# Kernel optimization log

Measured on AMD Instinct MI355X. Metric: run time of the kernel, lower is better.

Reference implementation:

```python
import jax, jax.numpy as jnp
import numpy as np

B, S = 16, 768
DCOG, DENV, NENV = 64, 32, 8
D, N, L, FF, NC = 512, 64, 6, 2048, 1
DIL = (1, 2, 4, 8)
EPS = 1e-5


def _layer_norm(x, g, b):
    m = x.mean(-1, keepdims=True)
    v = ((x - m) ** 2).mean(-1, keepdims=True)
    return (x - m) * jax.lax.rsqrt(v + EPS) * g + b


def _conv1d(x, w, b, d):
    # x: (B, D, S), w: (O, I, K); 'same' padding = (K-1)*d//2 = d for K=3
    y = jax.lax.conv_general_dilated(x, w, (1,), [(d, d)], rhs_dilation=(d,),
                                     dimension_numbers=('NCH', 'OIH', 'NCH'))
    return y + b[None, :, None]


def _combine(c1, c2):
    a1, b1 = c1
    a2, b2 = c2
    return a1 * a2, a2 * b1 + b2


def _forward(x_cog, cw1, cb1, cw2, cb2, env_emb, ew1, eb1, ew2, eb2,
             fw1, fb1, fw2, fb2, pos_enc, conv_w, conv_b, wm_w, wm_b,
             ssm_w, ssm_b, A_log, ffw1, ffb1, ffw2, ffb2,
             g1, be1, g2, be2, pw1, pb1, pw2, pb2, x_env):
    # Dual-channel feature processor (dropout = identity at eval)
    z = x_cog / jnp.maximum(jnp.linalg.norm(x_cog, axis=-1, keepdims=True), 1e-12)
    z = jnp.maximum(z @ cw1 + cb1, 0.0) @ cw2 + cb2
    e = env_emb[x_env].mean(-2)                      # (B,S,NENV,D) -> (B,S,D)
    e = jnp.maximum(e @ ew1 + eb1, 0.0) @ ew2 + eb2
    hf = jnp.concatenate([z, e], -1)
    hf = jnp.maximum(hf @ fw1 + fb1, 0.0) @ fw2 + fb2
    h = hf + pos_enc[:S][None]

    def layer_step(h, p):
        cw, cb, wmw, wmb, sw, sb, alog, w1, b1, w2, b2, g1_, be1_, g2_, be2_ = p
        # Multi-scale dilated conv
        xt = h.transpose(0, 2, 1)                    # (B, D, S)
        outs = [_conv1d(xt, cw[i], cb[i], DIL[i]) for i in range(4)]
        alpha = jax.nn.softmax(xt.mean(-1) @ wmw + wmb, -1)   # (B, 4)
        hm = sum(alpha[:, i, None, None] * outs[i] for i in range(4)).transpose(0, 2, 1)
        h1 = _layer_norm(hm + h, g1_, be1_)
        # Selective state-space (diagonal A), parallel associative scan
        proj = jnp.einsum('bsd,kdn->kbsn', h1, sw) + sb[:, None, None, :]
        delta, Bt, Ct = jax.nn.softplus(proj[0]), proj[1], proj[2]
        a = jnp.exp(alog[None, None, :] * delta)     # (B, S, N)
        bu = Bt * h1[..., :N]
        _, hs = jax.lax.associative_scan(_combine, (a, bu), axis=1)
        y = jnp.sum(Ct * hs, -1, keepdims=True)      # (B, S, 1)
        h2 = _layer_norm(y + h1, g2_, be2_)          # broadcast over D, as in torch
        return jnp.maximum(h2 @ w1 + b1, 0.0) @ w2 + b2 + h2, None

    h, _ = jax.lax.scan(layer_step, h, (conv_w, conv_b, wm_w, wm_b, ssm_w, ssm_b,
                                        A_log, ffw1, ffb1, ffw2, ffb2, g1, be1, g2, be2))
    hg = h.mean(1)                                   # adaptive avg pool over S
    return jnp.maximum(hg @ pw1 + pb1, 0.0) @ pw2 + pb2


def setup_inputs():
    ks = iter(jax.random.split(jax.random.key(0), 48))
    def rn(shape, s=0.02):
        return jax.random.normal(next(ks), shape, jnp.float32) * s
    return {
        'x_cog': rn((B, S, DCOG), 1.0),
        'cw1': rn((DCOG, D)), 'cb1': jnp.zeros(D), 'cw2': rn((D, D)), 'cb2': jnp.zeros(D),
        'env_emb': rn((DENV, D), 1.0),
        'ew1': rn((D, D)), 'eb1': jnp.zeros(D), 'ew2': rn((D, D)), 'eb2': jnp.zeros(D),
        'fw1': rn((2 * D, D)), 'fb1': jnp.zeros(D), 'fw2': rn((D, D)), 'fb2': jnp.zeros(D),
        'pos_enc': rn((1000, D), 1.0),
        'conv_w': rn((L, 4, D, D, 3)), 'conv_b': jnp.zeros((L, 4, D)),
        'wm_w': rn((L, D, 4)), 'wm_b': jnp.zeros((L, 4)),
        'ssm_w': rn((L, 3, D, N)), 'ssm_b': jnp.zeros((L, 3, N)),
        'A_log': -jnp.abs(rn((L, N), 1.0)),
        'ffw1': rn((L, D, FF)), 'ffb1': jnp.zeros((L, FF)),
        'ffw2': rn((L, FF, D)), 'ffb2': jnp.zeros((L, D)),
        'g1': jnp.ones((L, D)), 'be1': jnp.zeros((L, D)),
        'g2': jnp.ones((L, D)), 'be2': jnp.zeros((L, D)),
        'pw1': rn((D, D // 2)), 'pb1': jnp.zeros(D // 2),
        'pw2': rn((D // 2, NC)), 'pb2': jnp.zeros(NC),
        'x_env': jax.random.randint(next(ks), (B, S, NENV), 0, DENV, jnp.int32),
    }


def reference(x_cog, cw1, cb1, cw2, cb2, env_emb, ew1, eb1, ew2, eb2,
              fw1, fb1, fw2, fb2, pos_enc, conv_w, conv_b, wm_w, wm_b,
              ssm_w, ssm_b, A_log, ffw1, ffb1, ffw2, ffb2,
              g1, be1, g2, be2, pw1, pb1, pw2, pb2, x_env):
    return _forward(x_cog, cw1, cb1, cw2, cb2, env_emb, ew1, eb1, ew2, eb2,
                    fw1, fb1, fw2, fb2, pos_enc, conv_w, conv_b, wm_w, wm_b,
                    ssm_w, ssm_b, A_log, ffw1, ffb1, ffw2, ffb2,
                    g1, be1, g2, be2, pw1, pb1, pw2, pb2, x_env)
```

## Files before the change

### kernel.cpp

```cpp
#include <hip/hip_runtime.h>
#include <cstdint>
#include <cstddef>

namespace {

constexpr int B = 16, S = 768, BS = B * S, D = 512, FF = 2048, L = 6;
constexpr float EPS = 1e-5f;

typedef float f32x4 __attribute__((ext_vector_type(4)));
typedef _Float16 f16x8 __attribute__((ext_vector_type(8)));

__device__ __forceinline__ float wave_sum(float v) {
#pragma unroll
  for (int o = 32; o > 0; o >>= 1) v += __shfl_xor(v, o, 64);
  return v;
}

__device__ __forceinline__ short f16b(float x) {
  const _Float16 h = (_Float16)x;
  return __builtin_bit_cast(short, h);
}
__device__ __forceinline__ float h2f(short s) {
  return (float)__builtin_bit_cast(_Float16, s);
}

__device__ __forceinline__ void gload16(const void* g, void* l) {
  __builtin_amdgcn_global_load_lds(
      (const __attribute__((address_space(1))) void*)g,
      (__attribute__((address_space(3))) void*)l, 16, 0, 0);
}


template <bool RELU, bool PACK>
__global__ __launch_bounds__(256, 3) void gemm_h(
    const short* __restrict__ A, int lda, const short* __restrict__ Wt,
    int ldw, int Klen, const float* __restrict__ bias,
    short* __restrict__ ph, int ldp) {
  __shared__ alignas(16) short sAh[8192], sBh[8192];
  const int tid = threadIdx.x;
  const unsigned Nt = gridDim.x;
  const unsigned lin = blockIdx.y * Nt + blockIdx.x;
  const unsigned cpx = (Nt * gridDim.y) >> 3;
  const unsigned swz = (lin & 7) * cpx + (lin >> 3);
  const int bn = (int)(swz % Nt) * 128, bm = (int)(swz / Nt) * 128;
  const int wave = tid >> 6, lane = tid & 63;
  const int wr = (wave >> 1) * 64, wc = (wave & 1) * 64;
  const int lr = lane & 15, sl = lane >> 4;
  const short* Ab = A + (size_t)bm * lda;
  const short* Wb = Wt + (size_t)bn * ldw;
  f32x4 acc[4][4] = {};
  for (int kk = 0; kk < Klen; kk += 64) {
#pragma unroll
    for (int jj = 0; jj < 4; ++jj) {
      const int G = jj * 256 + tid;
      const int srow = G >> 3, sl0 = G & 7;
      const int gsl = sl0 ^ (srow & 7);
      const int dst = G * 8;
      gload16(Ab + (size_t)srow * lda + kk + gsl * 8, &sAh[dst]);
      gload16(Wb + (size_t)srow * ldw + kk + gsl * 8, &sBh[dst]);
    }
    __syncthreads();
#pragma unroll
    for (int ks = 0; ks < 2; ++ks) {
      f16x8 aH[4], bH[4];
#pragma unroll
      for (int m = 0; m < 4; ++m) {
        const int r = wr + m * 16 + lr;
        aH[m] = *(const f16x8*)&sAh[r * 64 + (((ks * 4 + sl) ^ (r & 7)) * 8)];
      }
#pragma unroll
      for (int n = 0; n < 4; ++n) {
        const int r = wc + n * 16 + lr;
        bH[n] = *(const f16x8*)&sBh[r * 64 + (((ks * 4 + sl) ^ (r & 7)) * 8)];
      }
#pragma unroll
      for (int m = 0; m < 4; ++m)
#pragma unroll
        for (int n = 0; n < 4; ++n)
          acc[m][n] = __builtin_amdgcn_mfma_f32_16x16x32_f16(aH[m], bH[n],
                                                             acc[m][n], 0, 0, 0);
    }
    __syncthreads();
  }
  const int r4 = sl * 4;
#pragma unroll
  for (int m = 0; m < 4; ++m) {
#pragma unroll
    for (int r = 0; r < 4; ++r) {
      const int mm = bm + wr + m * 16 + r4 + r;
#pragma unroll
      for (int n = 0; n < 4; ++n) {
        const int col = bn + wc + n * 16 + lr;
        float v = acc[m][n][r] + bias[col];
        if (RELU) v = fmaxf(v, 0.f);
        if (PACK) ph[(size_t)mm * ldp + col] = f16b(v);
      }
    }
  }
}

template <bool RELU, int RESM, bool PACK, bool CSUM>
__global__ __launch_bounds__(256, 3) void gemm_h64(
    const short* __restrict__ A, int lda, const short* __restrict__ Wt,
    int ldw, int Klen, const float* __restrict__ bias,
    const float* __restrict__ resid, const short* __restrict__ residS,
    int ldr, int rmod, short* __restrict__ ph, int ldp,
    float* __restrict__ part) {
  __shared__ alignas(16) short sAh[8192], sBh[4096];
  __shared__ float csLds[2][64];
  const int tid = threadIdx.x;
  const unsigned Nt = gridDim.x;
  const unsigned lin = blockIdx.y * Nt + blockIdx.x;
  const unsigned cpx = (Nt * gridDim.y) >> 3;
  const unsigned swz = (lin & 7) * cpx + (lin >> 3);
  const int bn = (int)(swz % Nt) * 64, bmt = (int)(swz / Nt);
  const int bm = bmt * 128;
  const int wave = tid >> 6, lane = tid & 63;
  const int wr = (wave >> 1) * 64, wc = (wave & 1) * 32;
  const int lr = lane & 15, sl = lane >> 4;
  const short* Ab = A + (size_t)bm * lda;
  const short* Wb = Wt + (size_t)bn * ldw;
  f32x4 acc[4][2] = {};
  for (int kk = 0; kk < Klen; kk += 64) {
#pragma unroll
    for (int jj = 0; jj < 4; ++jj) {
      const int G = jj * 256 + tid;
      const int srow = G >> 3, sl0 = G & 7;
      const int gsl = sl0 ^ (srow & 7);
      gload16(Ab + (size_t)srow * lda + kk + gsl * 8, &sAh[G * 8]);
    }
#pragma unroll
    for (int jj = 0; jj < 2; ++jj) {
      const int G = jj * 256 + tid;
      const int srow = G >> 3, sl0 = G & 7;
      const int gsl = sl0 ^ (srow & 7);
      gload16(Wb + (size_t)srow * ldw + kk + gsl * 8, &sBh[G * 8]);
    }
    __syncthreads();
#pragma unroll
    for (int ks = 0; ks < 2; ++ks) {
      f16x8 aH[4], bH[2];
#pragma unroll
      for (int m = 0; m < 4; ++m) {
        const int r = wr + m * 16 + lr;
        aH[m] = *(const f16x8*)&sAh[r * 64 + (((ks * 4 + sl) ^ (r & 7)) * 8)];
      }
#pragma unroll
      for (int n = 0; n < 2; ++n) {
        const int r = wc + n * 16 + lr;
        bH[n] = *(const f16x8*)&sBh[r * 64 + (((ks * 4 + sl) ^ (r & 7)) * 8)];
      }
#pragma unroll
      for (int m = 0; m < 4; ++m)
#pragma unroll
        for (int n = 0; n < 2; ++n)
          acc[m][n] = __builtin_amdgcn_mfma_f32_16x16x32_f16(aH[m], bH[n],
                                                             acc[m][n], 0, 0, 0);
    }
    __syncthreads();
  }
  const int r4 = sl * 4;
  float cs[2] = {0.f, 0.f};
#pragma unroll
  for (int m = 0; m < 4; ++m) {
#pragma unroll
    for (int r = 0; r < 4; ++r) {
      const int mm = bm + wr + m * 16 + r4 + r;
#pragma unroll
      for (int n = 0; n < 2; ++n) {
        const int col = bn + wc + n * 16 + lr;
        float v = acc[m][n][r] + bias[col];
        if (RELU) v = fmaxf(v, 0.f);
        if (RESM == 1) {
          const int rr = rmod ? (mm % rmod) : mm;
          v += resid[(size_t)rr * ldr + col];
        }
        if (RESM == 2) v += h2f(residS[(size_t)mm * ldr + col]);
        if (PACK) ph[(size_t)mm * ldp + col] = f16b(v);
        if (CSUM) cs[n] += v;
      }
    }
  }
  if constexpr (CSUM) {
#pragma unroll
    for (int n = 0; n < 2; ++n) {
      cs[n] += __shfl_xor(cs[n], 16, 64);
      cs[n] += __shfl_xor(cs[n], 32, 64);
    }
    if (sl == 0) {
      csLds[wave >> 1][wc + lr] = cs[0];
      csLds[wave >> 1][wc + 16 + lr] = cs[1];
    }
    __syncthreads();
    if (tid < 64)
      part[(size_t)bmt * 512 + bn + tid] = csLds[0][tid] + csLds[1][tid];
  }
}

__global__ __launch_bounds__(256, 3) void conv_zp_k(
    const short* __restrict__ hp, const short* __restrict__ wt8,
    const short* __restrict__ wmix, const float* __restrict__ alpha,
    const short* __restrict__ zpadS, short* __restrict__ P) {
  __shared__ alignas(16) short sAh[8192], sBh[8192];
  const int tid = threadIdx.x;
  const unsigned lin = blockIdx.x;
  const unsigned swz = (lin & 7) * 96 + (lin >> 3);
  const int zp = (int)(swz / 384);
  const unsigned rem = swz % 384;
  const int bn = (int)(rem & 3) * 128;
  const int bmt = (int)(rem >> 2);
  const int b = bmt / 6, s0 = (bmt % 6) * 128, gm0 = bmt * 128;
  const int wave = tid >> 6, lane = tid & 63;
  const int wr = (wave >> 1) * 64, wc = (wave & 1) * 64;
  const int lr = lane & 15, sl = lane >> 4;
  const short* hb = hp + (size_t)b * S * 512;
  f32x4 accF[4][4] = {};
#pragma unroll
  for (int zi = 0; zi < 2; ++zi) {
    const int z = zp * 2 + zi;
    const int dd = 1 << z;
    f32x4 acc[4][4] = {};
    for (int kk = 0; kk < 1024; kk += 64) {
      const int tap = kk >> 9;
      const int koff = kk & 511;
      const int off = tap ? dd : -dd;
#pragma unroll
      for (int jj = 0; jj < 4; ++jj) {
        const int G = jj * 256 + tid;
        const int srow = G >> 3, sl0 = G & 7;
        const int gsl = sl0 ^ (srow & 7);
        const int dst = G * 8;
        const int gs = s0 + srow + off;
        const bool inb = ((unsigned)gs < (unsigned)S);
        const short* aBase = hb + (size_t)gs * 512 + koff + gsl * 8;
        gload16(inb ? aBase : zpadS, &sAh[dst]);
        gload16(wt8 + ((size_t)((z * 2 + tap) * 512 + bn + srow)) * 512 +
                    koff + gsl * 8,
                &sBh[dst]);
      }
      __syncthreads();
#pragma unroll
      for (int ks = 0; ks < 2; ++ks) {
        f16x8 aH[4], bH[4];
#pragma unroll
        for (int m = 0; m < 4; ++m) {
          const int r = wr + m * 16 + lr;
          aH[m] =
              *(const f16x8*)&sAh[r * 64 + (((ks * 4 + sl) ^ (r & 7)) * 8)];
        }
#pragma unroll
        for (int n = 0; n < 4; ++n) {
          const int r = wc + n * 16 + lr;
          bH[n] =
              *(const f16x8*)&sBh[r * 64 + (((ks * 4 + sl) ^ (r & 7)) * 8)];
        }
#pragma unroll
        for (int m = 0; m < 4; ++m)
#pragma unroll
          for (int n = 0; n < 4; ++n)
            acc[m][n] = __builtin_amdgcn_mfma_f32_16x16x32_f16(
                aH[m], bH[n], acc[m][n], 0, 0, 0);
      }
      __syncthreads();
    }
    const float al = alpha[b * 4 + z];
#pragma unroll
    for (int m = 0; m < 4; ++m)
#pragma unroll
      for (int n = 0; n < 4; ++n)
#pragma unroll
        for (int r = 0; r < 4; ++r) accF[m][n][r] += al * acc[m][n][r];
  }
  const short* Wm = wmix + (size_t)b * 512 * 512;
  for (int kc = 0; kc < 256; kc += 64) {
    const int koff = zp * 256 + kc;
#pragma unroll
    for (int jj = 0; jj < 4; ++jj) {
      const int G = jj * 256 + tid;
      const int srow = G >> 3, sl0 = G & 7;
      const int gsl = sl0 ^ (srow & 7);
      const int dst = G * 8;
      gload16(hb + (size_t)(s0 + srow) * 512 + koff + gsl * 8, &sAh[dst]);
      gload16(Wm + (size_t)(bn + srow) * 512 + koff + gsl * 8, &sBh[dst]);
    }
    __syncthreads();
#pragma unroll
    for (int ks = 0; ks < 2; ++ks) {
      f16x8 aH[4], bH[4];
#pragma unroll
      for (int m = 0; m < 4; ++m) {
        const int r = wr + m * 16 + lr;
        aH[m] = *(const f16x8*)&sAh[r * 64 + (((ks * 4 + sl) ^ (r & 7)) * 8)];
      }
#pragma unroll
      for (int n = 0; n < 4; ++n) {
        const int r = wc + n * 16 + lr;
        bH[n] = *(const f16x8*)&sBh[r * 64 + (((ks * 4 + sl) ^ (r & 7)) * 8)];
      }
#pragma unroll
      for (int m = 0; m < 4; ++m)
#pragma unroll
        for (int n = 0; n < 4; ++n)
          accF[m][n] = __builtin_amdgcn_mfma_f32_16x16x32_f16(
              aH[m], bH[n], accF[m][n], 0, 0, 0);
    }
    __syncthreads();
  }
  short* Pz = P + (size_t)zp * ((size_t)BS * D);
  const int r4 = sl * 4;
#pragma unroll
  for (int m = 0; m < 4; ++m)
#pragma unroll
    for (int r = 0; r < 4; ++r) {
      const int mm = gm0 + wr + m * 16 + r4 + r;
#pragma unroll
      for (int n = 0; n < 4; ++n)
        Pz[(size_t)mm * D + bn + wc + n * 16 + lr] = f16b(accF[m][n][r]);
    }
}

__global__ __launch_bounds__(256) void ln3_k(
    const short* __restrict__ P0, const short* __restrict__ P1,
    const short* __restrict__ hpk, const float* __restrict__ cbmix,
    const float* __restrict__ g1, const float* __restrict__ b1,
    const float* __restrict__ g2, const float* __restrict__ b2,
    short* __restrict__ pout) {
  const int row = blockIdx.x * 4 + (threadIdx.x >> 6);
  const int lane = threadIdx.x & 63;
  const int bb = row / S;
  const size_t base = (size_t)row * D;
  float v[8];
  float s = 0.f;
#pragma unroll
  for (int j = 0; j < 8; ++j) {
    const int c = lane + 64 * j;
    v[j] = h2f(P0[base + c]) + h2f(P1[base + c]) + h2f(hpk[base + c]) +
           cbmix[(size_t)bb * D + c];
    s += v[j];
  }
  s = wave_sum(s);
  const float m1 = s * (1.f / D);
  float q = 0.f;
#pragma unroll
  for (int j = 0; j < 8; ++j) { const float d = v[j] - m1; q += d * d; }
  q = wave_sum(q);
  const float r1 = rsqrtf(q * (1.f / D) + EPS);
  float y[8];
  float s2 = 0.f;
#pragma unroll
  for (int j = 0; j < 8; ++j) {
    const int c = lane + 64 * j;
    y[j] = (v[j] - m1) * r1 * g1[c] + b1[c];
    s2 += y[j];
  }
  s2 = wave_sum(s2);
  const float m2 = s2 * (1.f / D);
  float q2 = 0.f;
#pragma unroll
  for (int j = 0; j < 8; ++j) { const float d = y[j] - m2; q2 += d * d; }
  q2 = wave_sum(q2);
  const float r2 = rsqrtf(q2 * (1.f / D) + EPS);
  short* prow = pout + base;
#pragma unroll
  for (int j = 0; j < 8; ++j) {
    const int c = lane + 64 * j;
    prow[c] = f16b((y[j] - m2) * r2 * g2[c] + b2[c]);
  }
}

__global__ __launch_bounds__(256) void pack_wt_k(const float* __restrict__ W,
                                                 short* __restrict__ out,
                                                 int K, int N) {
  __shared__ short t[64][68];
  const int n0 = blockIdx.x * 64, k0 = blockIdx.y * 64;
  const int ln = threadIdx.x & 63, w4 = threadIdx.x >> 6;
#pragma unroll
  for (int it = 0; it < 16; ++it) {
    const int kr = it * 4 + w4;
    t[kr][ln] = f16b(W[(size_t)(k0 + kr) * N + n0 + ln]);
  }
  __syncthreads();
#pragma unroll
  for (int it = 0; it < 16; ++it) {
    const int nr = it * 4 + w4;
    out[(size_t)(n0 + nr) * K + k0 + ln] = t[ln][nr];
  }
}

__global__ __launch_bounds__(256) void convprep_k(
    const float* __restrict__ cw, const float* __restrict__ alpha,
    short* __restrict__ out8, short* __restrict__ wm) {
  const int bid = blockIdx.x;
  if (bid < 8192) {
    const int idx = bid * 256 + threadIdx.x;
    const int c = idx & 511, o = (idx >> 9) & 511, seg = idx >> 18;
    const int z = seg >> 1, t = (seg & 1) * 2;
    out8[((size_t)seg * D + o) * D + c] =
        f16b(cw[(((size_t)z * D + o) * D + c) * 3 + t]);
  } else {
    __shared__ float sal[64];
    if (threadIdx.x < 64) sal[threadIdx.x] = alpha[threadIdx.x];
    __syncthreads();
    const int idx = (bid - 8192) * 256 + threadIdx.x;
    const int c = idx & 511, o = idx >> 9;
    float w[4];
#pragma unroll
    for (int z = 0; z < 4; ++z)
      w[z] = cw[(((size_t)z * D + o) * D + c) * 3 + 1];
#pragma unroll
    for (int b = 0; b < 16; ++b) {
      const float v = sal[b * 4 + 0] * w[0] + sal[b * 4 + 1] * w[1] +
                      sal[b * 4 + 2] * w[2] + sal[b * 4 + 3] * w[3];
      wm[((size_t)b * D + o) * D + c] = f16b(v);
    }
  }
}

__global__ __launch_bounds__(256) void zero_k(float* __restrict__ p) {
  p[threadIdx.x] = 0.f;
  p[threadIdx.x + 256] = 0.f;
}

__global__ __launch_bounds__(64) void alpha_k(const float* __restrict__ part,
                                              const float* __restrict__ wmw,
                                              const float* __restrict__ wmb,
                                              const float* __restrict__ cb,
                                              float* __restrict__ alpha,
                                              float* __restrict__ cbmix) {
  const int b = blockIdx.x, t = threadIdx.x;
  float p0 = 0, p1 = 0, p2 = 0, p3 = 0;
  for (int d = t; d < D; d += 64) {
    float xm = 0;
#pragma unroll
    for (int c = 0; c < 6; ++c) xm += part[((size_t)(b * 6 + c)) * D + d];
    xm *= (1.f / S);
    p0 += xm * wmw[d * 4 + 0];
    p1 += xm * wmw[d * 4 + 1];
    p2 += xm * wmw[d * 4 + 2];
    p3 += xm * wmw[d * 4 + 3];
  }
  p0 = wave_sum(p0); p1 = wave_sum(p1);
  p2 = wave_sum(p2); p3 = wave_sum(p3);
  const float l0 = p0 + wmb[0], l1 = p1 + wmb[1];
  const float l2 = p2 + wmb[2], l3 = p3 + wmb[3];
  const float mx = fmaxf(fmaxf(l0, l1), fmaxf(l2, l3));
  const float e0 = expf(l0 - mx), e1 = expf(l1 - mx);
  const float e2 = expf(l2 - mx), e3 = expf(l3 - mx);
  const float inv = 1.f / (e0 + e1 + e2 + e3);
  const float a0 = e0 * inv, a1 = e1 * inv, a2 = e2 * inv, a3 = e3 * inv;
  if (t == 0) {
    alpha[b * 4 + 0] = a0;
    alpha[b * 4 + 1] = a1;
    alpha[b * 4 + 2] = a2;
    alpha[b * 4 + 3] = a3;
  }
  for (int c = t; c < D; c += 64)
    cbmix[(size_t)b * D + c] =
        a0 * cb[c] + a1 * cb[D + c] + a2 * cb[2 * D + c] + a3 * cb[3 * D + c];
}

__global__ __launch_bounds__(256) void embed_k(const int* __restrict__ xe,
                                               const float* __restrict__ emb,
                                               short* __restrict__ out) {
  const int r = blockIdx.x;
  int idx[8];
#pragma unroll
  for (int j = 0; j < 8; ++j) idx[j] = xe[r * 8 + j];
  short* o = out + (size_t)r * 512;
  for (int d = threadIdx.x; d < D; d += 256) {
    float s = 0.f;
#pragma unroll
    for (int j = 0; j < 8; ++j) s += emb[(size_t)idx[j] * D + d];
    o[d] = f16b(s * 0.125f);
  }
}

__global__ __launch_bounds__(256) void norml2_k(const float* __restrict__ x,
                                                short* __restrict__ out) {
  const int r = blockIdx.x * 4 + (threadIdx.x >> 6);
  const int lane = threadIdx.x & 63;
  const float v = x[(size_t)r * 64 + lane];
  const float s = wave_sum(v * v);
  const float nrm = fmaxf(sqrtf(s), 1e-12f);
  out[(size_t)r * 64 + lane] = f16b(v / nrm);
}

__global__ __launch_bounds__(256) void head_k(
    const float* __restrict__ part, const float* __restrict__ pw1,
    const float* __restrict__ pb1, const float* __restrict__ pw2,
    const float* __restrict__ pb2, float* __restrict__ out) {
  __shared__ float hg[D];
  __shared__ float red[256];
  const int b = blockIdx.x, t = threadIdx.x;
  for (int d = t; d < D; d += 256) {
    float s = 0.f;
#pragma unroll
    for (int c = 0; c < 6; ++c) s += part[((size_t)(b * 6 + c)) * D + d];
    hg[d] = s * (1.f / S);
  }
  __syncthreads();
  float s = pb1[t];
  for (int d = 0; d < D; ++d) s = fmaf(hg[d], pw1[(size_t)d * 256 + t], s);
  s = fmaxf(s, 0.f);
  red[t] = s * pw2[t];
  __syncthreads();
  for (int o = 128; o > 0; o >>= 1) {
    if (t < o) red[t] += red[t + o];
    __syncthreads();
  }
  if (t == 0) out[b] = red[0] + pb2[0];
}

}

extern "C" void kernel_launch(void* const* d_in, const int* in_sizes, int n_in,
                              void* d_out, int out_size, void* d_ws,
                              size_t ws_size, hipStream_t stream) {
  const float* x_cog = (const float*)d_in[0];
  const float* cw1 = (const float*)d_in[1];
  const float* cb1 = (const float*)d_in[2];
  const float* cw2 = (const float*)d_in[3];
  const float* cb2 = (const float*)d_in[4];
  const float* env_emb = (const float*)d_in[5];
  const float* ew1 = (const float*)d_in[6];
  const float* eb1 = (const float*)d_in[7];
  const float* ew2 = (const float*)d_in[8];
  const float* eb2 = (const float*)d_in[9];
  const float* fw1 = (const float*)d_in[10];
  const float* fb1 = (const float*)d_in[11];
  const float* fw2 = (const float*)d_in[12];
  const float* fb2 = (const float*)d_in[13];
  const float* pos_enc = (const float*)d_in[14];
  const float* conv_w = (const float*)d_in[15];
  const float* conv_b = (const float*)d_in[16];
  const float* wm_w = (const float*)d_in[17];
  const float* wm_b = (const float*)d_in[18];
  const float* ffw1 = (const float*)d_in[22];
  const float* ffb1 = (const float*)d_in[23];
  const float* ffw2 = (const float*)d_in[24];
  const float* ffb2 = (const float*)d_in[25];
  const float* g1 = (const float*)d_in[26];
  const float* be1 = (const float*)d_in[27];
  const float* g2 = (const float*)d_in[28];
  const float* be2 = (const float*)d_in[29];
  const float* pw1 = (const float*)d_in[30];
  const float* pb1 = (const float*)d_in[31];
  const float* pw2 = (const float*)d_in[32];
  const float* pb2 = (const float*)d_in[33];
  const int* x_env = (const int*)d_in[34];
  float* out = (float*)d_out;

  float* ws = (float*)d_ws;
  float* PART2 = ws;
  float* ALPHAB = PART2 + 65536;
  float* ZPADF = ALPHAB + 64;
  float* CBMIX = ZPADF + 512;
  short* R = (short*)(CBMIX + 8192);
  short* WCONV8 = R;
  short* WFFP = R + 2097152;
  short* WMIX = R + 3145728;
  short* convPh = R + 7340032;
  short* APFF = R + 7340032;
  short* HPACK = R + 32505856;
  short* CONC = R;
  short* PK1 = R + 25165824;
  short* PK2 = R + 31457280;
  short* WPBF = R + 38797312;

  const dim3 blk(256);
  const dim3 gS(8, 96, 1);
  const dim3 gF(16, 96, 1);

  zero_k<<<1, blk, 0, stream>>>(ZPADF);

  norml2_k<<<BS / 4, blk, 0, stream>>>(x_cog, PK1);
  pack_wt_k<<<dim3(8, 1), blk, 0, stream>>>(cw1, WPBF, 64, 512);
  gemm_h64<true, 0, true, false><<<gS, blk, 0, stream>>>(
      PK1, 64, WPBF, 64, 64, cb1, nullptr, nullptr, 0, 0, PK2, 512, nullptr);
  pack_wt_k<<<dim3(8, 8), blk, 0, stream>>>(cw2, WPBF, 512, 512);
  gemm_h64<false, 0, true, false><<<gS, blk, 0, stream>>>(
      PK2, 512, WPBF, 512, 512, cb2, nullptr, nullptr, 0, 0, CONC, 2048,
      nullptr);
  embed_k<<<BS, blk, 0, stream>>>(x_env, env_emb, PK1);
  pack_wt_k<<<dim3(8, 8), blk, 0, stream>>>(ew1, WPBF, 512, 512);
  gemm_h64<true, 0, true, false><<<gS, blk, 0, stream>>>(
      PK1, 512, WPBF, 512, 512, eb1, nullptr, nullptr, 0, 0, PK2, 512,
      nullptr);
  pack_wt_k<<<dim3(8, 8), blk, 0, stream>>>(ew2, WPBF, 512, 512);
  gemm_h64<false, 0, true, false><<<gS, blk, 0, stream>>>(
      PK2, 512, WPBF, 512, 512, eb2, nullptr, nullptr, 0, 0, CONC + 512, 2048,
      nullptr);
  pack_wt_k<<<dim3(8, 16), blk, 0, stream>>>(fw1, WPBF, 1024, 512);
  gemm_h64<true, 0, true, false><<<gS, blk, 0, stream>>>(
      CONC, 2048, WPBF, 1024, 1024, fb1, nullptr, nullptr, 0, 0, PK1, 512,
      nullptr);
  pack_wt_k<<<dim3(8, 8), blk, 0, stream>>>(fw2, WPBF, 512, 512);
  gemm_h64<false, 1, true, true><<<gS, blk, 0, stream>>>(
      PK1, 512, WPBF, 512, 512, fb2, pos_enc, nullptr, 512, S, HPACK, 512,
      PART2);

  for (int l = 0; l < L; ++l) {
    const float* cwl = conv_w + (size_t)l * 4 * D * D * 3;
    alpha_k<<<B, dim3(64), 0, stream>>>(PART2, wm_w + (size_t)l * D * 4,
                                        wm_b + l * 4,
                                        conv_b + (size_t)l * 4 * D, ALPHAB,
                                        CBMIX);
    convprep_k<<<9216, blk, 0, stream>>>(cwl, ALPHAB, WCONV8, WMIX);
    conv_zp_k<<<768, blk, 0, stream>>>(HPACK, WCONV8, WMIX, ALPHAB,
                                       (const short*)ZPADF, convPh);
    ln3_k<<<BS / 4, blk, 0, stream>>>(convPh, convPh + (size_t)BS * D, HPACK,
                                      CBMIX, g1 + l * D, be1 + l * D,
                                      g2 + l * D, be2 + l * D, HPACK);
    pack_wt_k<<<dim3(32, 8), blk, 0, stream>>>(ffw1 + (size_t)l * D * FF,
                                               WFFP, 512, 2048);
    gemm_h<true, true><<<gF, blk, 0, stream>>>(HPACK, 512, WFFP, 512, 512,
                                               ffb1 + (size_t)l * FF, APFF,
                                               2048);
    pack_wt_k<<<dim3(8, 32), blk, 0, stream>>>(ffw2 + (size_t)l * FF * D,
                                               WFFP, 2048, 512);
    gemm_h64<false, 2, true, true><<<gS, blk, 0, stream>>>(
        APFF, 2048, WFFP, 2048, 2048, ffb2 + (size_t)l * D, nullptr, HPACK,
        512, 0, HPACK, 512, PART2);
  }

  head_k<<<B, blk, 0, stream>>>(PART2, pw1, pb1, pw2, pb2, out);
}
```

Before: 1.129 ms.

## Batch weight packing upfront, widen GEMM K-tiles, and restructure conv tiling

All FFN and conv weights for every layer are now packed to fp16 in two kernels before the layer loop, replacing the per-layer pack launches. The conv kernel no longer splits dilations across blocks: each block covers all four dilations for a 128x64 tile with a 128-wide K step, so the second partial-sum buffer and its read in the layernorm kernel go away. The 64-wide-tile GEMM gains a BK template parameter and uses 128 for most calls, halving barrier count. The trade-off is more LDS per block, which may reduce occupancy, and a larger upfront packing cost.

```diff
diff --git a/kernel.cpp b/kernel.cpp
--- a/kernel.cpp
+++ b/kernel.cpp
@@ -99,14 +99,18 @@
   }
 }
 
-template <bool RELU, int RESM, bool PACK, bool CSUM>
+template <bool RELU, int RESM, bool PACK, bool CSUM, int BK>
 __global__ __launch_bounds__(256, 3) void gemm_h64(
     const short* __restrict__ A, int lda, const short* __restrict__ Wt,
     int ldw, int Klen, const float* __restrict__ bias,
     const float* __restrict__ resid, const short* __restrict__ residS,
     int ldr, int rmod, short* __restrict__ ph, int ldp,
     float* __restrict__ part) {
-  __shared__ alignas(16) short sAh[8192], sBh[4096];
+  constexpr int GPR = BK / 8;
+  constexpr int AR = 128 * GPR / 256;
+  constexpr int BR = 64 * GPR / 256;
+  constexpr int KS = BK / 32;
+  __shared__ alignas(16) short sAh[128 * BK], sBh[64 * BK];
   __shared__ float csLds[2][64];
   const int tid = threadIdx.x;
   const unsigned Nt = gridDim.x;
@@ -121,34 +125,36 @@
   const short* Ab = A + (size_t)bm * lda;
   const short* Wb = Wt + (size_t)bn * ldw;
   f32x4 acc[4][2] = {};
-  for (int kk = 0; kk < Klen; kk += 64) {
-#pragma unroll
-    for (int jj = 0; jj < 4; ++jj) {
+  for (int kk = 0; kk < Klen; kk += BK) {
+#pragma unroll
+    for (int jj = 0; jj < AR; ++jj) {
       const int G = jj * 256 + tid;
-      const int srow = G >> 3, sl0 = G & 7;
-      const int gsl = sl0 ^ (srow & 7);
+      const int srow = G / GPR, sl0 = G % GPR;
+      const int gsl = sl0 ^ (srow & (GPR - 1));
       gload16(Ab + (size_t)srow * lda + kk + gsl * 8, &sAh[G * 8]);
     }
 #pragma unroll
-    for (int jj = 0; jj < 2; ++jj) {
+    for (int jj = 0; jj < BR; ++jj) {
       const int G = jj * 256 + tid;
-      const int srow = G >> 3, sl0 = G & 7;
-      const int gsl = sl0 ^ (srow & 7);
+      const int srow = G / GPR, sl0 = G % GPR;
+      const int gsl = sl0 ^ (srow & (GPR - 1));
       gload16(Wb + (size_t)srow * ldw + kk + gsl * 8, &sBh[G * 8]);
     }
     __syncthreads();
 #pragma unroll
-    for (int ks = 0; ks < 2; ++ks) {
+    for (int ks = 0; ks < KS; ++ks) {
       f16x8 aH[4], bH[2];
 #pragma unroll
       for (int m = 0; m < 4; ++m) {
         const int r = wr + m * 16 + lr;
-        aH[m] = *(const f16x8*)&sAh[r * 64 + (((ks * 4 + sl) ^ (r & 7)) * 8)];
+        aH[m] = *(const f16x8*)
+            &sAh[r * BK + (((ks * 4 + sl) ^ (r & (GPR - 1))) * 8)];
       }
 #pragma unroll
       for (int n = 0; n < 2; ++n) {
         const int r = wc + n * 16 + lr;
-        bH[n] = *(const f16x8*)&sBh[r * 64 + (((ks * 4 + sl) ^ (r & 7)) * 8)];
+        bH[n] = *(const f16x8*)
+            &sBh[r * BK + (((ks * 4 + sl) ^ (r & (GPR - 1))) * 8)];
       }
 #pragma unroll
       for (int m = 0; m < 4; ++m)
@@ -201,63 +207,65 @@
     const short* __restrict__ hp, const short* __restrict__ wt8,
     const short* __restrict__ wmix, const float* __restrict__ alpha,
     const short* __restrict__ zpadS, short* __restrict__ P) {
-  __shared__ alignas(16) short sAh[8192], sBh[8192];
+  __shared__ alignas(16) short sAh[16384], sBh[8192];
   const int tid = threadIdx.x;
   const unsigned lin = blockIdx.x;
   const unsigned swz = (lin & 7) * 96 + (lin >> 3);
-  const int zp = (int)(swz / 384);
-  const unsigned rem = swz % 384;
-  const int bn = (int)(rem & 3) * 128;
-  const int bmt = (int)(rem >> 2);
+  const int bn = (int)(swz & 7) * 64;
+  const int bmt = (int)(swz >> 3);
   const int b = bmt / 6, s0 = (bmt % 6) * 128, gm0 = bmt * 128;
   const int wave = tid >> 6, lane = tid & 63;
-  const int wr = (wave >> 1) * 64, wc = (wave & 1) * 64;
+  const int wr = (wave >> 1) * 64, wc = (wave & 1) * 32;
   const int lr = lane & 15, sl = lane >> 4;
   const short* hb = hp + (size_t)b * S * 512;
-  f32x4 accF[4][4] = {};
-#pragma unroll
-  for (int zi = 0; zi < 2; ++zi) {
-    const int z = zp * 2 + zi;
+  f32x4 accF[4][2] = {};
+#pragma unroll
+  for (int z = 0; z < 4; ++z) {
     const int dd = 1 << z;
-    f32x4 acc[4][4] = {};
-    for (int kk = 0; kk < 1024; kk += 64) {
+    f32x4 acc[4][2] = {};
+    for (int kk = 0; kk < 1024; kk += 128) {
       const int tap = kk >> 9;
       const int koff = kk & 511;
       const int off = tap ? dd : -dd;
 #pragma unroll
-      for (int jj = 0; jj < 4; ++jj) {
+      for (int jj = 0; jj < 8; ++jj) {
         const int G = jj * 256 + tid;
-        const int srow = G >> 3, sl0 = G & 7;
-        const int gsl = sl0 ^ (srow & 7);
-        const int dst = G * 8;
+        const int srow = G >> 4, sl0 = G & 15;
+        const int gsl = sl0 ^ (srow & 15);
         const int gs = s0 + srow + off;
         const bool inb = ((unsigned)gs < (unsigned)S);
         const short* aBase = hb + (size_t)gs * 512 + koff + gsl * 8;
-        gload16(inb ? aBase : zpadS, &sAh[dst]);
+        gload16(inb ? aBase : zpadS, &sAh[G * 8]);
+      }
+#pragma unroll
+      for (int jj = 0; jj < 4; ++jj) {
+        const int G = jj * 256 + tid;
+        const int srow = G >> 4, sl0 = G & 15;
+        const int gsl = sl0 ^ (srow & 15);
         gload16(wt8 + ((size_t)((z * 2 + tap) * 512 + bn + srow)) * 512 +
                     koff + gsl * 8,
-                &sBh[dst]);
+                &sBh[G * 8]);
       }
       __syncthreads();
 #pragma unroll
-      for (int ks = 0; ks < 2; ++ks) {
-        f16x8 aH[4], bH[4];
+      for (int ks = 0; ks < 4; ++ks) {
+        f16x8 aH[4], bH[2];
 #pragma unroll
         for (int m = 0; m < 4; ++m) {
           const int r = wr + m * 16 + lr;
-          aH[m] =
-              *(const f16x8*)&sAh[r * 64 + (((ks * 4 + sl) ^ (r & 7)) * 8)];
+          aH[m] = *(const f16x8*)
+              &sAh[r * 128 + (((ks * 4 + sl) ^ (r & 15)) * 8)];
         }
 #pragma unroll
-        for (int n = 0; n < 4; ++n) {
+        for (int n = 0; n < 2; ++n) {
           const int r = wc + n * 16 + lr;
-          bH[n] =
-              *(const f16x8*)&sBh[r * 64 + (((ks * 4 + sl) ^ (r & 7)) * 8)];
+          bH[n] = *(const f16x8*)
+              &sBh[r * 128 + (((ks * 4 + sl) ^ (r & 15)) * 8)];
         }
 #pragma unroll
         for (int m = 0; m < 4; ++m)
 #pragma unroll
-          for (int n = 0; n < 4; ++n)
+          for (int n = 0; n < 2; ++n)
             acc[m][n] = __builtin_amdgcn_mfma_f32_16x16x32_f16(
                 aH[m], bH[n], acc[m][n], 0, 0, 0);
       }
@@ -267,46 +275,51 @@
 #pragma unroll
     for (int m = 0; m < 4; ++m)
 #pragma unroll
-      for (int n = 0; n < 4; ++n)
+      for (int n = 0; n < 2; ++n)
 #pragma unroll
         for (int r = 0; r < 4; ++r) accF[m][n][r] += al * acc[m][n][r];
   }
   const short* Wm = wmix + (size_t)b * 512 * 512;
-  for (int kc = 0; kc < 256; kc += 64) {
-    const int koff = zp * 256 + kc;
+  for (int kc = 0; kc < 512; kc += 128) {
+#pragma unroll
+    for (int jj = 0; jj < 8; ++jj) {
+      const int G = jj * 256 + tid;
+      const int srow = G >> 4, sl0 = G & 15;
+      const int gsl = sl0 ^ (srow & 15);
+      gload16(hb + (size_t)(s0 + srow) * 512 + kc + gsl * 8, &sAh[G * 8]);
+    }
 #pragma unroll
     for (int jj = 0; jj < 4; ++jj) {
       const int G = jj * 256 + tid;
-      const int srow = G >> 3, sl0 = G & 7;
-      const int gsl = sl0 ^ (srow & 7);
-      const int dst = G * 8;
-      gload16(hb + (size_t)(s0 + srow) * 512 + koff + gsl * 8, &sAh[dst]);
-      gload16(Wm + (size_t)(bn + srow) * 512 + koff + gsl * 8, &sBh[dst]);
-    }
-    __syncthreads();
-#pragma unroll
-    for (int ks = 0; ks < 2; ++ks) {
-      f16x8 aH[4], bH[4];
+      const int srow = G >> 4, sl0 = G & 15;
+      const int gsl = sl0 ^ (srow & 15);
+      gload16(Wm + (size_t)(bn + srow) * 512 + kc + gsl * 8, &sBh[G * 8]);
+    }
+    __syncthreads();
+#pragma unroll
+    for (int ks = 0; ks < 4; ++ks) {
+      f16x8 aH[4], bH[2];
 #pragma unroll
       for (int m = 0; m < 4; ++m) {
         const int r = wr + m * 16 + lr;
-        aH[m] = *(const f16x8*)&sAh[r * 64 + (((ks * 4 + sl) ^ (r & 7)) * 8)];
-      }
-#pragma unroll
-      for (int n = 0; n < 4; ++n) {
+        aH[m] =
+            *(const f16x8*)&sAh[r * 128 + (((ks * 4 + sl) ^ (r & 15)) * 8)];
+      }
+#pragma unroll
+      for (int n = 0; n < 2; ++n) {
         const int r = wc + n * 16 + lr;
-        bH[n] = *(const f16x8*)&sBh[r * 64 + (((ks * 4 + sl) ^ (r & 7)) * 8)];
+        bH[n] =
+            *(const f16x8*)&sBh[r * 128 + (((ks * 4 + sl) ^ (r & 15)) * 8)];
       }
 #pragma unroll
       for (int m = 0; m < 4; ++m)
 #pragma unroll
-        for (int n = 0; n < 4; ++n)
+        for (int n = 0; n < 2; ++n)
           accF[m][n] = __builtin_amdgcn_mfma_f32_16x16x32_f16(
               aH[m], bH[n], accF[m][n], 0, 0, 0);
     }
     __syncthreads();
   }
-  short* Pz = P + (size_t)zp * ((size_t)BS * D);
   const int r4 = sl * 4;
 #pragma unroll
   for (int m = 0; m < 4; ++m)
@@ -314,17 +327,16 @@
     for (int r = 0; r < 4; ++r) {
       const int mm = gm0 + wr + m * 16 + r4 + r;
 #pragma unroll
-      for (int n = 0; n < 4; ++n)
-        Pz[(size_t)mm * D + bn + wc + n * 16 + lr] = f16b(accF[m][n][r]);
+      for (int n = 0; n < 2; ++n)
+        P[(size_t)mm * D + bn + wc + n * 16 + lr] = f16b(accF[m][n][r]);
     }
 }
 
 __global__ __launch_bounds__(256) void ln3_k(
-    const short* __restrict__ P0, const short* __restrict__ P1,
-    const short* __restrict__ hpk, const float* __restrict__ cbmix,
-    const float* __restrict__ g1, const float* __restrict__ b1,
-    const float* __restrict__ g2, const float* __restrict__ b2,
-    short* __restrict__ pout) {
+    const short* __restrict__ P0, const short* __restrict__ hpk,
+    const float* __restrict__ cbmix, const float* __restrict__ g1,
+    const float* __restrict__ b1, const float* __restrict__ g2,
+    const float* __restrict__ b2, short* __restrict__ pout) {
   const int row = blockIdx.x * 4 + (threadIdx.x >> 6);
   const int lane = threadIdx.x & 63;
   const int bb = row / S;
@@ -334,8 +346,7 @@
 #pragma unroll
   for (int j = 0; j < 8; ++j) {
     const int c = lane + 64 * j;
-    v[j] = h2f(P0[base + c]) + h2f(P1[base + c]) + h2f(hpk[base + c]) +
-           cbmix[(size_t)bb * D + c];
+    v[j] = h2f(P0[base + c]) + h2f(hpk[base + c]) + cbmix[(size_t)bb * D + c];
     s += v[j];
   }
   s = wave_sum(s);
@@ -368,51 +379,75 @@
   }
 }
 
+__device__ __forceinline__ void pack_tile(const float* __restrict__ W,
+                                          short* __restrict__ out, int K,
+                                          int N, int n0, int k0) {
+  __shared__ short t[64][68];
+  const int ln = threadIdx.x & 63, w4 = threadIdx.x >> 6;
+#pragma unroll
+  for (int it = 0; it < 16; ++it) {
+    const int kr = it * 4 + w4;
+    t[kr][ln] = f16b(W[(size_t)(k0 + kr) * N + n0 + ln]);
+  }
+  __syncthreads();
+#pragma unroll
+  for (int it = 0; it < 16; ++it) {
+    const int nr = it * 4 + w4;
+    out[(size_t)(n0 + nr) * K + k0 + ln] = t[ln][nr];
+  }
+}
+
 __global__ __launch_bounds__(256) void pack_wt_k(const float* __restrict__ W,
                                                  short* __restrict__ out,
                                                  int K, int N) {
-  __shared__ short t[64][68];
-  const int n0 = blockIdx.x * 64, k0 = blockIdx.y * 64;
-  const int ln = threadIdx.x & 63, w4 = threadIdx.x >> 6;
-#pragma unroll
-  for (int it = 0; it < 16; ++it) {
-    const int kr = it * 4 + w4;
-    t[kr][ln] = f16b(W[(size_t)(k0 + kr) * N + n0 + ln]);
-  }
+  pack_tile(W, out, K, N, blockIdx.x * 64, blockIdx.y * 64);
+}
+
+__global__ __launch_bounds__(256) void pack_ff_all_k(
+    const float* __restrict__ ffw1, const float* __restrict__ ffw2,
+    short* __restrict__ outAll) {
+  const int bid = blockIdx.x;
+  const int l = bid >> 9;
+  const int r = bid & 511;
+  if (r < 256) {
+    pack_tile(ffw1 + (size_t)l * D * FF, outAll + (size_t)l * 2097152, 512,
+              2048, (r & 31) * 64, (r >> 5) * 64);
+  } else {
+    const int r2 = r - 256;
+    pack_tile(ffw2 + (size_t)l * FF * D,
+              outAll + (size_t)l * 2097152 + 1048576, 2048, 512,
+              (r2 & 7) * 64, (r2 >> 3) * 64);
+  }
+}
+
+__global__ __launch_bounds__(256) void pack_conv8_all_k(
+    const float* __restrict__ cw, short* __restrict__ out) {
+  const size_t idx = (size_t)blockIdx.x * 256 + threadIdx.x;
+  const int c = (int)(idx & 511);
+  const int o = (int)((idx >> 9) & 511);
+  const int seg = (int)((idx >> 18) & 7);
+  const int l = (int)(idx >> 21);
+  const int z = seg >> 1, t = (seg & 1) * 2;
+  out[idx] = f16b(cw[((size_t)l * 4 * D * D + ((size_t)z * D + o) * D + c) * 3 + t]);
+}
+
+__global__ __launch_bounds__(256) void wmix_k(const float* __restrict__ cw,
+                                              const float* __restrict__ alpha,
+                                              short* __restrict__ wm) {
+  __shared__ float sal[64];
+  if (threadIdx.x < 64) sal[threadIdx.x] = alpha[threadIdx.x];
   __syncthreads();
-#pragma unroll
-  for (int it = 0; it < 16; ++it) {
-    const int nr = it * 4 + w4;
-    out[(size_t)(n0 + nr) * K + k0 + ln] = t[ln][nr];
-  }
-}
-
-__global__ __launch_bounds__(256) void convprep_k(
-    const float* __restrict__ cw, const float* __restrict__ alpha,
-    short* __restrict__ out8, short* __restrict__ wm) {
-  const int bid = blockIdx.x;
-  if (bid < 8192) {
-    const int idx = bid * 256 + threadIdx.x;
-    const int c = idx & 511, o = (idx >> 9) & 511, seg = idx >> 18;
-    const int z = seg >> 1, t = (seg & 1) * 2;
-    out8[((size_t)seg * D + o) * D + c] =
-        f16b(cw[(((size_t)z * D + o) * D + c) * 3 + t]);
-  } else {
-    __shared__ float sal[64];
-    if (threadIdx.x < 64) sal[threadIdx.x] = alpha[threadIdx.x];
-    __syncthreads();
-    const int idx = (bid - 8192) * 256 + threadIdx.x;
-    const int c = idx & 511, o = idx >> 9;
-    float w[4];
-#pragma unroll
-    for (int z = 0; z < 4; ++z)
-      w[z] = cw[(((size_t)z * D + o) * D + c) * 3 + 1];
-#pragma unroll
-    for (int b = 0; b < 16; ++b) {
-      const float v = sal[b * 4 + 0] * w[0] + sal[b * 4 + 1] * w[1] +
-                      sal[b * 4 + 2] * w[2] + sal[b * 4 + 3] * w[3];
-      wm[((size_t)b * D + o) * D + c] = f16b(v);
-    }
+  const int idx = blockIdx.x * 256 + threadIdx.x;
+  const int c = idx & 511, o = idx >> 9;
+  float w[4];
+#pragma unroll
+  for (int z = 0; z < 4; ++z)
+    w[z] = cw[(((size_t)z * D + o) * D + c) * 3 + 1];
+#pragma unroll
+  for (int b = 0; b < 16; ++b) {
+    const float v = sal[b * 4 + 0] * w[0] + sal[b * 4 + 1] * w[1] +
+                    sal[b * 4 + 2] * w[2] + sal[b * 4 + 3] * w[3];
+    wm[((size_t)b * D + o) * D + c] = f16b(v);
   }
 }
 
@@ -556,46 +591,48 @@
   float* ZPADF = ALPHAB + 64;
   float* CBMIX = ZPADF + 512;
   short* R = (short*)(CBMIX + 8192);
-  short* WCONV8 = R;
-  short* WFFP = R + 2097152;
-  short* WMIX = R + 3145728;
-  short* convPh = R + 7340032;
-  short* APFF = R + 7340032;
-  short* HPACK = R + 32505856;
-  short* CONC = R;
-  short* PK1 = R + 25165824;
-  short* PK2 = R + 31457280;
-  short* WPBF = R + 38797312;
+  short* WFFALL = R;
+  short* WC8ALL = R + 12582912;
+  short* WMIX = R + 25165824;
+  short* convPh = R + 29360128;
+  short* HPACK = R + 35651584;
+  short* APFF = R + 41943040;
+  short* CONC = APFF;
+  short* PK1 = R + 67108864;
+  short* PK2 = R + 73400320;
+  short* WPBF = R + 79691776;
 
   const dim3 blk(256);
   const dim3 gS(8, 96, 1);
   const dim3 gF(16, 96, 1);
 
   zero_k<<<1, blk, 0, stream>>>(ZPADF);
+  pack_ff_all_k<<<3072, blk, 0, stream>>>(ffw1, ffw2, WFFALL);
+  pack_conv8_all_k<<<49152, blk, 0, stream>>>(conv_w, WC8ALL);
 
   norml2_k<<<BS / 4, blk, 0, stream>>>(x_cog, PK1);
   pack_wt_k<<<dim3(8, 1), blk, 0, stream>>>(cw1, WPBF, 64, 512);
-  gemm_h64<true, 0, true, false><<<gS, blk, 0, stream>>>(
+  gemm_h64<true, 0, true, false, 64><<<gS, blk, 0, stream>>>(
       PK1, 64, WPBF, 64, 64, cb1, nullptr, nullptr, 0, 0, PK2, 512, nullptr);
   pack_wt_k<<<dim3(8, 8), blk, 0, stream>>>(cw2, WPBF, 512, 512);
-  gemm_h64<false, 0, true, false><<<gS, blk, 0, stream>>>(
+  gemm_h64<false, 0, true, false, 128><<<gS, blk, 0, stream>>>(
       PK2, 512, WPBF, 512, 512, cb2, nullptr, nullptr, 0, 0, CONC, 2048,
       nullptr);
   embed_k<<<BS, blk, 0, stream>>>(x_env, env_emb, PK1);
   pack_wt_k<<<dim3(8, 8), blk, 0, stream>>>(ew1, WPBF, 512, 512);
-  gemm_h64<true, 0, true, false><<<gS, blk, 0, stream>>>(
+  gemm_h64<true, 0, true, false, 128><<<gS, blk, 0, stream>>>(
       PK1, 512, WPBF, 512, 512, eb1, nullptr, nullptr, 0, 0, PK2, 512,
       nullptr);
   pack_wt_k<<<dim3(8, 8), blk, 0, stream>>>(ew2, WPBF, 512, 512);
-  gemm_h64<false, 0, true, false><<<gS, blk, 0, stream>>>(
+  gemm_h64<false, 0, true, false, 128><<<gS, blk, 0, stream>>>(
       PK2, 512, WPBF, 512, 512, eb2, nullptr, nullptr, 0, 0, CONC + 512, 2048,
       nullptr);
   pack_wt_k<<<dim3(8, 16), blk, 0, stream>>>(fw1, WPBF, 1024, 512);
-  gemm_h64<true, 0, true, false><<<gS, blk, 0, stream>>>(
+  gemm_h64<true, 0, true, false, 128><<<gS, blk, 0, stream>>>(
       CONC, 2048, WPBF, 1024, 1024, fb1, nullptr, nullptr, 0, 0, PK1, 512,
       nullptr);
   pack_wt_k<<<dim3(8, 8), blk, 0, stream>>>(fw2, WPBF, 512, 512);
-  gemm_h64<false, 1, true, true><<<gS, blk, 0, stream>>>(
+  gemm_h64<false, 1, true, true, 128><<<gS, blk, 0, stream>>>(
       PK1, 512, WPBF, 512, 512, fb2, pos_enc, nullptr, 512, S, HPACK, 512,
       PART2);
 
@@ -605,22 +642,19 @@
                                         wm_b + l * 4,
                                         conv_b + (size_t)l * 4 * D, ALPHAB,
                                         CBMIX);
-    convprep_k<<<9216, blk, 0, stream>>>(cwl, ALPHAB, WCONV8, WMIX);
-    conv_zp_k<<<768, blk, 0, stream>>>(HPACK, WCONV8, WMIX, ALPHAB,
-                                       (const short*)ZPADF, convPh);
-    ln3_k<<<BS / 4, blk, 0, stream>>>(convPh, convPh + (size_t)BS * D, HPACK,
-                                      CBMIX, g1 + l * D, be1 + l * D,
-                                      g2 + l * D, be2 + l * D, HPACK);
-    pack_wt_k<<<dim3(32, 8), blk, 0, stream>>>(ffw1 + (size_t)l * D * FF,
-                                               WFFP, 512, 2048);
-    gemm_h<true, true><<<gF, blk, 0, stream>>>(HPACK, 512, WFFP, 512, 512,
-                                               ffb1 + (size_t)l * FF, APFF,
-                                               2048);
-    pack_wt_k<<<dim3(8, 32), blk, 0, stream>>>(ffw2 + (size_t)l * FF * D,
-                                               WFFP, 2048, 512);
-    gemm_h64<false, 2, true, true><<<gS, blk, 0, stream>>>(
-        APFF, 2048, WFFP, 2048, 2048, ffb2 + (size_t)l * D, nullptr, HPACK,
-        512, 0, HPACK, 512, PART2);
+    wmix_k<<<1024, blk, 0, stream>>>(cwl, ALPHAB, WMIX);
+    conv_zp_k<<<768, blk, 0, stream>>>(HPACK, WC8ALL + (size_t)l * 2097152,
+                                       WMIX, ALPHAB, (const short*)ZPADF,
+                                       convPh);
+    ln3_k<<<BS / 4, blk, 0, stream>>>(convPh, HPACK, CBMIX, g1 + l * D,
+                                      be1 + l * D, g2 + l * D, be2 + l * D,
+                                      HPACK);
+    gemm_h<true, true><<<gF, blk, 0, stream>>>(
+        HPACK, 512, WFFALL + (size_t)l * 2097152, 512, 512,
+        ffb1 + (size_t)l * FF, APFF, 2048);
+    gemm_h64<false, 2, true, true, 128><<<gS, blk, 0, stream>>>(
+        APFF, 2048, WFFALL + (size_t)l * 2097152 + 1048576, 2048, 2048,
+        ffb2 + (size_t)l * D, nullptr, HPACK, 512, 0, HPACK, 512, PART2);
   }
 
   head_k<<<B, blk, 0, stream>>>(PART2, pw1, pb1, pw2, pb2, out);
```

Measured after the change: 1.245 ms. 10.3% more time.
